# Optimization experiments

Measured on AMD Instinct MI355X. Metric: run time of the kernel, lower is better.

Reference implementation:

```python
import jax, jax.numpy as jnp
import numpy as np

NEG = -1e30  # log-space 'zero'


def _lse3(a, b, c):
    # numerically stable logsumexp of three [B,L] arrays, NEG acts as -inf
    m = jnp.maximum(jnp.maximum(a, b), c)
    valid = m > NEG / 2
    m_safe = jnp.where(valid, m, 0.0)
    s = jnp.exp(a - m_safe) + jnp.exp(b - m_safe) + jnp.exp(c - m_safe)
    # add 1 where invalid so log() stays finite (result is masked anyway)
    return jnp.where(valid, m_safe + jnp.log(s + (~valid)), NEG)


def _lse2(a, b):
    m = jnp.maximum(a, b)
    valid = m > NEG / 2
    m_safe = jnp.where(valid, m, 0.0)
    s = jnp.exp(a - m_safe) + jnp.exp(b - m_safe)
    return jnp.where(valid, m_safe + jnp.log(s + (~valid)), NEG)


def ctc_loss(log_probs, targets, input_lengths, target_lengths):
    # log_probs: [T,B,C] already log-softmaxed; blank=0; reduction='mean'; zero_infinity
    T, B, C = log_probs.shape
    S = targets.shape[0] // B  # equal target lengths -> reshape concatenated targets
    tgt = targets.reshape(B, S)
    L = 2 * S + 1
    # extended label sequence: blank, l1, blank, l2, ..., blank
    ext = jnp.zeros((B, L), dtype=tgt.dtype).at[:, 1::2].set(tgt)
    # emissions gathered at extended labels: [T,B,L]
    emit = log_probs[:, jnp.arange(B)[:, None], ext]

    # skip transition (l-2 -> l) allowed iff ext[l] != blank and ext[l] != ext[l-2]
    skip_ok = jnp.concatenate(
        [jnp.zeros((B, 2), bool), (ext[:, 2:] != 0) & (ext[:, 2:] != ext[:, :-2])],
        axis=1,
    )

    def shift(a, n):
        return jnp.pad(a, ((0, 0), (n, 0)), constant_values=NEG)[:, :L]

    alpha0 = (
        jnp.full((B, L), NEG, log_probs.dtype)
        .at[:, 0].set(emit[0, :, 0])
        .at[:, 1].set(emit[0, :, 1])
    )

    def step(alpha, xs):
        t, emit_t = xs
        a1 = shift(alpha, 1)
        a2 = jnp.where(skip_ok, shift(alpha, 2), NEG)
        new = _lse3(alpha, a1, a2) + emit_t
        # freeze alpha once past each sample's input length
        new = jnp.where((t < input_lengths)[:, None], new, alpha)
        return new, None

    alpha, _ = jax.lax.scan(step, alpha0, (jnp.arange(1, T), emit[1:]))

    b_idx = jnp.arange(B)
    hi = 2 * target_lengths  # last blank position
    ll = _lse2(alpha[b_idx, hi], alpha[b_idx, hi - 1])
    loss = jnp.where(ll > NEG / 2, -ll, 0.0)  # zero_infinity=True
    return jnp.mean(loss / target_lengths.astype(log_probs.dtype))


def setup_inputs() -> dict:
    key = jax.random.key(0)
    k1, k2 = jax.random.split(key)
    T, B, C, S = 1024, 128, 256, 64
    logits = jax.random.normal(k1, (T, B, C), jnp.float32)
    log_probs = jax.nn.log_softmax(logits, axis=-1)
    targets = jax.random.randint(k2, (B * S,), 1, C)  # blank=0 excluded
    input_lengths = jnp.full((B,), T, jnp.int32)
    target_lengths = jnp.full((B,), S, jnp.int32)
    return {
        "log_probs": log_probs,
        "targets": targets,
        "input_lengths": input_lengths,
        "target_lengths": target_lengths,
    }


def reference(log_probs, targets, input_lengths, target_lengths):
    return ctc_loss(log_probs, targets, input_lengths, target_lengths)
```

## Files before the change

### kernel.cpp

```cpp
#include <hip/hip_runtime.h>


#define NEGV (-1e30f)
#define NEGH (-5e29f)

constexpr int T_  = 1024;
constexpr int C_  = 256;
constexpr int CH  = 64;
constexpr int NCH = T_ / CH;

__device__ __forceinline__ float lse2f(float x, float y) {
    float m = fmaxf(x, y);
    float s = __expf(x - m) + __expf(y - m);
    float r = m + __logf(s);
    return (m > NEGH) ? r : NEGV;
}

__device__ __forceinline__ double dshr1(double x) {
    int lo = __double2loint(x), hi = __double2hiint(x);
    int plo = __builtin_amdgcn_update_dpp(0, lo, 0x138, 0xf, 0xf, false);
    int phi = __builtin_amdgcn_update_dpp(0, hi, 0x138, 0xf, 0xf, false);
    return __hiloint2double(phi, plo);
}

template <int CTRL>
__device__ __forceinline__ int dpp_imaxstep(int x) {
    int r = __builtin_amdgcn_update_dpp(x, x, CTRL, 0xf, 0xf, false);
    return max(x, r);
}

__global__ __launch_bounds__(128) void ctc_alpha_kernel(
    const float* __restrict__ lp,
    const int* __restrict__ targets,
    const int* __restrict__ in_len,
    const int* __restrict__ tgt_len,
    float* __restrict__ partial,
    int B, int S)
{
    __shared__ float2 stage[2][CH][64];
    __shared__ float sh[132];

    const int b    = blockIdx.x;
    const int tid  = threadIdx.x;
    const int wave = tid >> 6;
    const int lane = tid & 63;
    const int BC   = B * C_;
    const float* rowb = lp + (size_t)b * C_;

    int my_tgt = (lane < S) ? targets[b * S + lane] : 0;
    int prev_tgt = __shfl_up(my_tgt, 1);
    const bool skip = (lane > 0) && (my_tgt != prev_tgt) && (my_tgt != 0);
    const int ilen = in_len[b];

    double pa = 0.0, pb = 0.0, pc = 0.0;
    int es = 0;
    if (wave == 0 && lane == 0) {
        pa = (double)__expf(rowb[0]);
        pb = (double)__expf(rowb[my_tgt]);
    }

    if (wave == 1) {
#pragma unroll
        for (int r = 0; r < CH; ++r) {
            const size_t off = (size_t)(1 + r) * BC;
            float g  = rowb[off + my_tgt];
            float bl = rowb[off];
            stage[0][r][lane] = make_float2(__expf(g), __expf(bl));
        }
    }
    __syncthreads();

    for (int kc = 0; kc < NCH; ++kc) {
        if (wave == 1) {
            if (kc + 1 < NCH) {
                const int bufn = (kc + 1) & 1;
                const int t0 = 1 + (kc + 1) * CH;
#pragma unroll
                for (int r = 0; r < CH; ++r) {
                    int t = t0 + r;
                    t = (t > T_ - 1) ? (T_ - 1) : t;
                    const size_t off = (size_t)t * BC;
                    float g  = rowb[off + my_tgt];
                    float bl = rowb[off];
                    stage[bufn][r][lane] = make_float2(__expf(g), __expf(bl));
                }
            }
        } else {
            const int buf = kc & 1;
            const int t0  = 1 + kc * CH;
#pragma unroll
            for (int r = 0; r < CH; ++r) {
                const int t = t0 + r;
                if (t < ilen) {
                    float2 em = stage[buf][r][lane];
                    double eml = (double)em.x;
                    double ebl = (double)em.y;
                    double pprev = dshr1(pb);
                    double ts = pa + pprev;
                    double nb = (pb + (skip ? ts : pa)) * eml;
                    double na = ts * ebl;
                    double nc = (pc + pb) * ebl;
                    pa = na; pb = nb; pc = nc;
                    if ((r & 31) == 31) {
                        int h = max(max(__double2hiint(pa), __double2hiint(pb)),
                                    __double2hiint(pc));
                        h = dpp_imaxstep<0x111>(h);
                        h = dpp_imaxstep<0x112>(h);
                        h = dpp_imaxstep<0x114>(h);
                        h = dpp_imaxstep<0x118>(h);
                        h = dpp_imaxstep<0x142>(h);
                        h = dpp_imaxstep<0x143>(h);
                        int hm = __builtin_amdgcn_readlane(h, 63);
                        int e = ((hm >> 20) & 0x7ff) - 1023;
                        pa = ldexp(pa, -e);
                        pb = ldexp(pb, -e);
                        pc = ldexp(pc, -e);
                        es += e;
                    }
                }
            }
        }
        __syncthreads();
    }

    if (wave == 0) {
        const double lses = (double)es * 0.6931471805599453;
        auto logp = [&](double p) -> float {
            if (p == 0.0) return NEGV;
            int hi = __double2hiint(p), lo = __double2loint(p);
            int E = ((hi >> 20) & 0x7ff) - 1023;
            int hin = (hi & (int)0x800FFFFF) | (1023 << 20);
            double m = __hiloint2double(hin, lo);
            return (float)(__logf((float)m) + ((double)E * 0.6931471805599453 + lses));
        };
        sh[2 * lane]     = logp(pa);
        sh[2 * lane + 1] = logp(pb);
        if (lane == 63) sh[128] = logp(pc);
    }
    __syncthreads();
    if (tid == 0) {
        int tl = tgt_len[b];
        int hi2 = 2 * tl;
        float ll = lse2f(sh[hi2], sh[hi2 - 1]);
        float loss = (ll > NEGH) ? -ll : 0.f;
        partial[b] = loss / (float)tl;
    }
}

__global__ __launch_bounds__(128) void ctc_reduce_kernel(
    const float* __restrict__ partial, float* __restrict__ out, int B)
{
    float v = 0.f;
    for (int j = threadIdx.x; j < B; j += 128) v += partial[j];
#pragma unroll
    for (int off = 32; off > 0; off >>= 1)
        v += __shfl_down(v, off);
    __shared__ float ws[2];
    if ((threadIdx.x & 63) == 0) ws[threadIdx.x >> 6] = v;
    __syncthreads();
    if (threadIdx.x == 0) out[0] = (ws[0] + ws[1]) / (float)B;
}

extern "C" void kernel_launch(void* const* d_in, const int* in_sizes, int n_in,
                              void* d_out, int out_size, void* d_ws, size_t ws_size,
                              hipStream_t stream)
{
    const float* lp      = (const float*)d_in[0];
    const int*   targets = (const int*)d_in[1];
    const int*   il      = (const int*)d_in[2];
    const int*   tl      = (const int*)d_in[3];
    const int B = in_sizes[2];
    const int S = in_sizes[1] / B;

    float* partial = (float*)d_ws;

    ctc_alpha_kernel<<<B, 128, 0, stream>>>(lp, targets, il, tl, partial, B, S);
    ctc_reduce_kernel<<<1, 128, 0, stream>>>(partial, (float*)d_out, B);
}
```

Before: 240.7 us.

## Split emission prefetch across two producer waves and software-pipeline LDS reads

Raises the block from two to three waves so that two producer waves each gather and exponentiate half of the next chunk's emissions, halving the producer's per-chunk latency. The consumer wave now prefetches LDS emission values four steps ahead in registers. It also replaces the skip select with an FMA by a 0/1 double. The aim is to keep the serial alpha recurrence from stalling on the producer or on LDS latency, at the cost of an extra wave per block and more registers.

Measured after the change: 201.0 us. -16.5%, faster.

```diff
diff --git a/kernel.cpp b/kernel.cpp
--- a/kernel.cpp
+++ b/kernel.cpp
@@ -8,6 +8,7 @@
 constexpr int C_  = 256;
 constexpr int CH  = 64;
 constexpr int NCH = T_ / CH;
+constexpr int PD  = 4;
 
 __device__ __forceinline__ float lse2f(float x, float y) {
     float m = fmaxf(x, y);
@@ -29,7 +30,7 @@
     return max(x, r);
 }
 
-__global__ __launch_bounds__(128) void ctc_alpha_kernel(
+__global__ __launch_bounds__(192) void ctc_alpha_kernel(
     const float* __restrict__ lp,
     const int* __restrict__ targets,
     const int* __restrict__ in_len,
@@ -50,6 +51,7 @@
     int my_tgt = (lane < S) ? targets[b * S + lane] : 0;
     int prev_tgt = __shfl_up(my_tgt, 1);
     const bool skip = (lane > 0) && (my_tgt != prev_tgt) && (my_tgt != 0);
+    const double skipd = skip ? 1.0 : 0.0;
     const int ilen = in_len[b];
 
     double pa = 0.0, pb = 0.0, pc = 0.0;
@@ -59,63 +61,73 @@
         pb = (double)__expf(rowb[my_tgt]);
     }
 
-    if (wave == 1) {
+    if (wave >= 1) {
+        const int r0 = (wave - 1) * (CH / 2);
 #pragma unroll
-        for (int r = 0; r < CH; ++r) {
-            const size_t off = (size_t)(1 + r) * BC;
+        for (int r = 0; r < CH / 2; ++r) {
+            int t = 1 + r0 + r;
+            const size_t off = (size_t)t * BC;
             float g  = rowb[off + my_tgt];
             float bl = rowb[off];
-            stage[0][r][lane] = make_float2(__expf(g), __expf(bl));
+            stage[0][r0 + r][lane] = make_float2(__expf(g), __expf(bl));
         }
     }
     __syncthreads();
 
     for (int kc = 0; kc < NCH; ++kc) {
-        if (wave == 1) {
+        if (wave >= 1) {
             if (kc + 1 < NCH) {
                 const int bufn = (kc + 1) & 1;
-                const int t0 = 1 + (kc + 1) * CH;
+                const int r0 = (wave - 1) * (CH / 2);
+                const int t0 = 1 + (kc + 1) * CH + r0;
 #pragma unroll
-                for (int r = 0; r < CH; ++r) {
+                for (int r = 0; r < CH / 2; ++r) {
                     int t = t0 + r;
                     t = (t > T_ - 1) ? (T_ - 1) : t;
                     const size_t off = (size_t)t * BC;
                     float g  = rowb[off + my_tgt];
                     float bl = rowb[off];
-                    stage[bufn][r][lane] = make_float2(__expf(g), __expf(bl));
+                    stage[bufn][r0 + r][lane] = make_float2(__expf(g), __expf(bl));
                 }
             }
         } else {
-            const int buf = kc & 1;
-            const int t0  = 1 + kc * CH;
+            const int t0 = 1 + kc * CH;
+            if (t0 < ilen) {
+                const float2* sb = &stage[kc & 1][0][lane];
+                float2 f0 = sb[0 * 64];
+                float2 f1 = sb[1 * 64];
+                float2 f2 = sb[2 * 64];
+                float2 f3 = sb[3 * 64];
 #pragma unroll
-            for (int r = 0; r < CH; ++r) {
-                const int t = t0 + r;
-                if (t < ilen) {
-                    float2 em = stage[buf][r][lane];
-                    double eml = (double)em.x;
-                    double ebl = (double)em.y;
-                    double pprev = dshr1(pb);
-                    double ts = pa + pprev;
-                    double nb = (pb + (skip ? ts : pa)) * eml;
-                    double na = ts * ebl;
-                    double nc = (pc + pb) * ebl;
-                    pa = na; pb = nb; pc = nc;
-                    if ((r & 31) == 31) {
-                        int h = max(max(__double2hiint(pa), __double2hiint(pb)),
-                                    __double2hiint(pc));
-                        h = dpp_imaxstep<0x111>(h);
-                        h = dpp_imaxstep<0x112>(h);
-                        h = dpp_imaxstep<0x114>(h);
-                        h = dpp_imaxstep<0x118>(h);
-                        h = dpp_imaxstep<0x142>(h);
-                        h = dpp_imaxstep<0x143>(h);
-                        int hm = __builtin_amdgcn_readlane(h, 63);
-                        int e = ((hm >> 20) & 0x7ff) - 1023;
-                        pa = ldexp(pa, -e);
-                        pb = ldexp(pb, -e);
-                        pc = ldexp(pc, -e);
-                        es += e;
+                for (int r = 0; r < CH; ++r) {
+                    float2 cur = f0;
+                    f0 = f1; f1 = f2; f2 = f3;
+                    if (r + PD < CH) f3 = sb[(r + PD) * 64];
+                    if (t0 + r < ilen) {
+                        double eml = (double)cur.x;
+                        double ebl = (double)cur.y;
+                        double pprev = dshr1(pb);
+                        double u  = fma(skipd, pprev, pa);
+                        double nb = (pb + u) * eml;
+                        double na = (pa + pprev) * ebl;
+                        double nc = (pc + pb) * ebl;
+                        pa = na; pb = nb; pc = nc;
+                        if ((r & 31) == 31) {
+                            int h = max(max(__double2hiint(pa), __double2hiint(pb)),
+                                        __double2hiint(pc));
+                            h = dpp_imaxstep<0x111>(h);
+                            h = dpp_imaxstep<0x112>(h);
+                            h = dpp_imaxstep<0x114>(h);
+                            h = dpp_imaxstep<0x118>(h);
+                            h = dpp_imaxstep<0x142>(h);
+                            h = dpp_imaxstep<0x143>(h);
+                            int hm = __builtin_amdgcn_readlane(h, 63);
+                            int e = ((hm >> 20) & 0x7ff) - 1023;
+                            pa = ldexp(pa, -e);
+                            pb = ldexp(pb, -e);
+                            pc = ldexp(pc, -e);
+                            es += e;
+                        }
                     }
                 }
             }
@@ -174,6 +186,6 @@
 
     float* partial = (float*)d_ws;
 
-    ctc_alpha_kernel<<<B, 128, 0, stream>>>(lp, targets, il, tl, partial, B, S);
+    ctc_alpha_kernel<<<B, 192, 0, stream>>>(lp, targets, il, tl, partial, B, S);
     ctc_reduce_kernel<<<1, 128, 0, stream>>>(partial, (float*)d_out, B);
 }
```
